# Performance work log

Hardware: AMD Instinct MI355X
Metric: run time of the kernel (lower is better)

Reference implementation:

```python
import jax, jax.numpy as jnp
import numpy as np

B, N, D_IN, D_OUT = 4, 2048, 1024, 1024


def setup_inputs() -> dict:
    key = jax.random.key(0)
    kx, kq, kk, kv = jax.random.split(key, 4)
    x = jax.random.normal(kx, (B, N, D_IN), dtype=jnp.float32)
    # torch Linear(d_in, d_out, bias=False): y = x @ W.T, W ~ U(-1/sqrt(d_in), 1/sqrt(d_in)).
    # Store as [d_in, d_out] so y = x @ W.
    bound = 1.0 / np.sqrt(D_IN)
    Wq = jax.random.uniform(kq, (D_IN, D_OUT), jnp.float32, -bound, bound)
    Wk = jax.random.uniform(kk, (D_IN, D_OUT), jnp.float32, -bound, bound)
    Wv = jax.random.uniform(kv, (D_IN, D_OUT), jnp.float32, -bound, bound)
    return {"x": x, "Wq": Wq, "Wk": Wk, "Wv": Wv}


def reference(x, Wq, Wk, Wv):
    # x: [B, N, d_in]
    q = jnp.einsum("bnd,de->bne", x, Wq)  # [B, N, d_out]
    k = jnp.einsum("bnd,de->bne", x, Wk)
    v = jnp.einsum("bnd,de->bne", x, Wv)
    n = x.shape[1]
    scores = jnp.einsum("bqe,bke->bqk", q, k)  # [B, N, N]
    causal = jnp.triu(jnp.ones((n, n), dtype=bool), k=1)  # True above diagonal -> masked
    scores = jnp.where(causal, -jnp.inf, scores)
    scale = 1.0 / jnp.sqrt(jnp.asarray(k.shape[-1], dtype=scores.dtype))
    weights = jax.nn.softmax(scores * scale, axis=-1)
    # dropout with drop_rate=0.0 is identity
    return jnp.einsum("bqk,bke->bqe", weights, v)  # [B, N, d_out]
```

## Files before the change

kernel.cpp:

```cpp
#include <hip/hip_runtime.h>

typedef float  f4v  __attribute__((ext_vector_type(4)));
typedef short  s8v  __attribute__((ext_vector_type(8)));

__device__ __forceinline__ ushort f2b(float f) {
    union { float f; unsigned int u; } v; v.f = f;
    unsigned int u = v.u;
    u += 0x7fffu + ((u >> 16) & 1u);
    return (ushort)(u >> 16);
}
__device__ __forceinline__ float b2f(ushort u) {
    union { unsigned int u; float f; } v; v.u = ((unsigned int)u) << 16;
    return v.f;
}

__device__ __forceinline__ void async16(const ushort* g, ushort* ldsp) {
    __builtin_amdgcn_global_load_lds(
        (const __attribute__((address_space(1))) unsigned int*)g,
        (__attribute__((address_space(3))) unsigned int*)ldsp, 16, 0, 0);
}

__global__ __launch_bounds__(256) void cast_f32_bf16(const float* __restrict__ in,
                                                     ushort* __restrict__ out,
                                                     float* __restrict__ l, int n4) {
    int i = blockIdx.x * 256 + threadIdx.x;
    if (i < 8192) l[i] = 0.f;
    if (i < n4) {
        float4 f = ((const float4*)in)[i];
        ushort4 o;
        o.x = f2b(f.x); o.y = f2b(f.y); o.z = f2b(f.z); o.w = f2b(f.w);
        ((ushort4*)out)[i] = o;
    }
}

__global__ __launch_bounds__(256) void transpose_cast(const float* __restrict__ w0,
                                                      const float* __restrict__ w1,
                                                      const float* __restrict__ w2,
                                                      ushort* __restrict__ out) {
    __shared__ float tile[32][33];
    const float* W = (blockIdx.z == 0) ? w0 : (blockIdx.z == 1 ? w1 : w2);
    ushort* O = out + (size_t)blockIdx.z * (1024u * 1024u);
    int x0 = blockIdx.x * 32, y0 = blockIdx.y * 32;
    int tx = threadIdx.x, ty = threadIdx.y;
    for (int i = 0; i < 4; i++)
        tile[ty + i * 8][tx] = W[(size_t)(y0 + ty + i * 8) * 1024 + x0 + tx];
    __syncthreads();
    for (int i = 0; i < 4; i++)
        O[(size_t)(x0 + ty + i * 8) * 1024 + y0 + tx] = f2b(tile[tx][ty + i * 8]);
}

#define GEMM_KLOOP64_N64(ArowP_, BrowP_, strideA_, strideB_, K0_, KMAX_)              \
    for (int k0 = (K0_); k0 < (KMAX_); k0 += 64) {                                    \
        async16(ArowP_ + k0, sAw);                                                    \
        async16(ArowP_ + k0 + 16 * (strideA_), sAw + 16 * 32);                        \
        async16(ArowP_ + k0 + 32, sAw + 4096);                                        \
        async16(ArowP_ + k0 + 32 + 16 * (strideA_), sAw + 4096 + 16 * 32);            \
        async16(BrowP_ + k0, sBw);                                                    \
        async16(BrowP_ + k0 + 32, sBw + 2048);                                        \
        __syncthreads();                                                              \
        for (int s = 0; s < 2; s++) {                                                 \
            s8v af[4], bf[2];                                                         \
            for (int mi = 0; mi < 4; mi++)                                            \
                af[mi] = *(const s8v*)&sA[s * 4096 + (wm + mi * 16 + l16) * 32 + quad * 8]; \
            for (int ni = 0; ni < 2; ni++)                                            \
                bf[ni] = *(const s8v*)&sB[s * 2048 + (wn + ni * 16 + l16) * 32 + quad * 8]; \
            for (int mi = 0; mi < 4; mi++)                                            \
                for (int ni = 0; ni < 2; ni++)                                        \
                    acc[mi][ni] = __builtin_amdgcn_mfma_f32_16x16x32_bf16(            \
                        af[mi], bf[ni], acc[mi][ni], 0, 0, 0);                        \
        }                                                                             \
        __syncthreads();                                                              \
    }

#define GEMM_PREAMBLE_N64                                                             \
    const int tid = threadIdx.x;                                                      \
    const int w = tid >> 6, lane = tid & 63, quad = lane >> 4, l16 = lane & 15;       \
    const int wm = (w >> 1) * 64, wn = (w & 1) * 32;                                  \
    f4v acc[4][2];                                                                    \
    for (int mi = 0; mi < 4; mi++)                                                    \
        for (int ni = 0; ni < 2; ni++) acc[mi][ni] = 0;                               \
    ushort* sAw = &sA[(w * 32) * 32];                                                 \
    ushort* sBw = &sB[(w * 16) * 32];

__global__ __launch_bounds__(512, 2) void gemm_qkv(const ushort* __restrict__ A,
                                                   const ushort* __restrict__ Wt,
                                                   ushort* __restrict__ q,
                                                   ushort* __restrict__ k,
                                                   ushort* __restrict__ vt) {
    constexpr int K = 1024;
    extern __shared__ ushort lds[];

    const int L = blockIdx.x;
    const int xcd = L & 7, idx = L >> 3;
    const int ci = xcd >> 1, cj = xcd & 1;
    const int mo = idx / 12, no = idx - mo * 12;
    const int mt = ci * 8 + mo;
    const int ntile = cj * 12 + no;
    const int z = ntile >> 3;
    const int m0 = mt * 256;
    const int n0 = (ntile & 7) * 128;
    const ushort* Bt = Wt + (size_t)z * 1024 * 1024;

    const int tid = threadIdx.x;
    const int w = tid >> 6, lane = tid & 63, quad = lane >> 4, l16 = lane & 15;
    const int wm = (w >> 1) * 64, wn = (w & 1) * 64;

    ushort* a0 = lds;           ushort* b0 = lds + 16384;
    ushort* a1 = lds + 24576;   ushort* b1 = lds + 40960;
    ushort* a2 = lds + 49152;   ushort* b2 = lds + 65536;

    const int lr = lane >> 3;
    const int lc8 = (lane & 7) ^ lr;
    const ushort* Ab = A  + (size_t)(m0 + w * 8 + lr) * K + lc8 * 8;
    const ushort* Bb = Bt + (size_t)(n0 + w * 8 + lr) * K + lc8 * 8;
    const int dW = w * 512;

    f4v acc[4][4];
    #pragma unroll
    for (int mi = 0; mi < 4; mi++)
        #pragma unroll
        for (int ni = 0; ni < 4; ni++) acc[mi][ni] = 0;

    #pragma unroll
    for (int a = 0; a < 4; a++) async16(Ab + (size_t)a * 64 * K,      a0 + a * 4096 + dW);
    #pragma unroll
    for (int b = 0; b < 2; b++) async16(Bb + (size_t)b * 64 * K,      b0 + b * 4096 + dW);
    #pragma unroll
    for (int a = 0; a < 4; a++) async16(Ab + (size_t)a * 64 * K + 64, a1 + a * 4096 + dW);
    #pragma unroll
    for (int b = 0; b < 2; b++) async16(Bb + (size_t)b * 64 * K + 64, b1 + b * 4096 + dW);
    asm volatile("s_waitcnt vmcnt(6)" ::: "memory");
    asm volatile("s_barrier" ::: "memory");

    for (int t = 0; t < 16; ++t) {
        const int k2 = (t + 2) * 64;
        s8v af[4][2], bf[2][2];

        #pragma unroll
        for (int mi = 0; mi < 4; mi++)
            #pragma unroll
            for (int s = 0; s < 2; s++)
                af[mi][s] = *(const s8v*)&a0[(wm + mi * 16 + l16) * 64 +
                                             (((s * 4 + quad) ^ (l16 & 7)) * 8)];
        #pragma unroll
        for (int ni = 0; ni < 2; ni++)
            #pragma unroll
            for (int s = 0; s < 2; s++)
                bf[ni][s] = *(const s8v*)&b0[(wn + ni * 16 + l16) * 64 +
                                             (((s * 4 + quad) ^ (l16 & 7)) * 8)];
        if (t < 14) {
            async16(Ab + (size_t)0 * 64 * K + k2, a2 + 0 * 4096 + dW);
            async16(Ab + (size_t)1 * 64 * K + k2, a2 + 1 * 4096 + dW);
            async16(Ab + (size_t)2 * 64 * K + k2, a2 + 2 * 4096 + dW);
        }
        asm volatile("s_barrier" ::: "memory");
        __builtin_amdgcn_s_setprio(1);
        #pragma unroll
        for (int mi = 0; mi < 4; mi++)
            #pragma unroll
            for (int ni = 0; ni < 2; ni++)
                #pragma unroll
                for (int s = 0; s < 2; s++)
                    acc[mi][ni] = __builtin_amdgcn_mfma_f32_16x16x32_bf16(
                        af[mi][s], bf[ni][s], acc[mi][ni], 0, 0, 0);
        __builtin_amdgcn_s_setprio(0);
        asm volatile("s_barrier" ::: "memory");

        #pragma unroll
        for (int ni = 0; ni < 2; ni++)
            #pragma unroll
            for (int s = 0; s < 2; s++)
                bf[ni][s] = *(const s8v*)&b0[(wn + (ni + 2) * 16 + l16) * 64 +
                                             (((s * 4 + quad) ^ (l16 & 7)) * 8)];
        if (t < 14) {
            async16(Ab + (size_t)3 * 64 * K + k2, a2 + 3 * 4096 + dW);
            async16(Bb + (size_t)0 * 64 * K + k2, b2 + 0 * 4096 + dW);
            async16(Bb + (size_t)1 * 64 * K + k2, b2 + 1 * 4096 + dW);
        }
        asm volatile("s_barrier" ::: "memory");
        __builtin_amdgcn_s_setprio(1);
        #pragma unroll
        for (int mi = 0; mi < 4; mi++)
            #pragma unroll
            for (int ni = 0; ni < 2; ni++)
                #pragma unroll
                for (int s = 0; s < 2; s++)
                    acc[mi][ni + 2] = __builtin_amdgcn_mfma_f32_16x16x32_bf16(
                        af[mi][s], bf[ni][s], acc[mi][ni + 2], 0, 0, 0);
        __builtin_amdgcn_s_setprio(0);

        if (t < 14)       asm volatile("s_waitcnt vmcnt(6)" ::: "memory");
        else if (t == 14) asm volatile("s_waitcnt vmcnt(0)" ::: "memory");
        asm volatile("s_barrier" ::: "memory");

        ushort* ta = a0; a0 = a1; a1 = a2; a2 = ta;
        ushort* tb = b0; b0 = b1; b1 = b2; b2 = tb;
    }

    if (z < 2) {
        ushort* C = (z == 0) ? q : k;
        #pragma unroll
        for (int mi = 0; mi < 4; mi++)
            #pragma unroll
            for (int ni = 0; ni < 4; ni++) {
                int row = m0 + wm + mi * 16 + quad * 4;
                int col = n0 + wn + ni * 16 + l16;
                f4v v = acc[mi][ni];
                #pragma unroll
                for (int rr = 0; rr < 4; rr++)
                    C[(size_t)(row + rr) * 1024 + col] = f2b(v[rr]);
            }
    } else {
        #pragma unroll
        for (int mi = 0; mi < 4; mi++)
            #pragma unroll
            for (int ni = 0; ni < 4; ni++) {
                int row = m0 + wm + mi * 16 + quad * 4;
                int col = n0 + wn + ni * 16 + l16;
                f4v v = acc[mi][ni];
                int b = row >> 11, tok = row & 2047;
                ushort4 pk;
                pk.x = f2b(v[0]); pk.y = f2b(v[1]); pk.z = f2b(v[2]); pk.w = f2b(v[3]);
                *(ushort4*)&vt[(size_t)b * (1024u * 2048u) + (size_t)col * 2048 + tok] = pk;
            }
    }
}

__global__ __launch_bounds__(256) void sgemm_qk(const ushort* __restrict__ Q,
                                                const ushort* __restrict__ Km,
                                                ushort* __restrict__ E,
                                                float* __restrict__ l) {
    constexpr int K = 1024;
    __shared__ ushort sA[2 * 4096];
    __shared__ ushort sB[2 * 2048];
    const int L = blockIdx.x;
    const int t = (L & 7) * 136 + (L >> 3);
    const int b = t / 272;
    const int tt = t - b * 272;
    int mt = 0;
    while ((mt + 1) * (mt + 2) <= tt) mt++;
    const int nt = tt - mt * (mt + 1);
    const ushort* A  = Q  + (size_t)b * 2048 * 1024;
    const ushort* Bt = Km + (size_t)b * 2048 * 1024;
    ushort* C = E + (size_t)b * 2048 * 2048;
    float* lb = l + (size_t)b * 2048;
    const int m0 = mt * 128, n0 = nt * 64;
    GEMM_PREAMBLE_N64
    const ushort* ArowP = A + (size_t)(m0 + w * 32 + (lane >> 2)) * K + (lane & 3) * 8;
    const ushort* BrowP = Bt + (size_t)(n0 + w * 16 + (lane >> 2)) * K + (lane & 3) * 8;
    GEMM_KLOOP64_N64(ArowP, BrowP, K, K, 0, K)

    for (int mi = 0; mi < 4; mi++) {
        for (int rr = 0; rr < 4; rr++) {
            const int row = m0 + wm + mi * 16 + quad * 4 + rr;
            float s = 0.f;
            for (int ni = 0; ni < 2; ni++) {
                int col = n0 + wn + ni * 16 + l16;
                float e = (col <= row) ? __expf(acc[mi][ni][rr] * 0.03125f) : 0.f;
                ushort eb = f2b(e);
                C[(size_t)row * 2048 + col] = eb;
                s += b2f(eb);
            }
            s += __shfl_xor(s, 1);
            s += __shfl_xor(s, 2);
            s += __shfl_xor(s, 4);
            s += __shfl_xor(s, 8);
            if (l16 == 0) atomicAdd(&lb[row], s);
        }
    }
}

__global__ __launch_bounds__(256) void gemm_pv(const ushort* __restrict__ Em,
                                               const ushort* __restrict__ Vt,
                                               const float* __restrict__ l,
                                               float* __restrict__ Out) {
    __shared__ ushort sA[2 * 4096];
    __shared__ ushort sB[2 * 2048];
    const int L = blockIdx.x;
    const int t = (L & 7) * 128 + (L >> 3);
    const int b = t >> 8;
    const int r = t & 255;
    const int qq = r >> 4;
    const int nt = r & 15;
    const int mt = (qq & 1) ? (qq >> 1) : (15 - (qq >> 1));
    const ushort* A  = Em + (size_t)b * 2048 * 2048;
    const ushort* Bt = Vt + (size_t)b * 1024 * 2048;
    const float* lb = l + (size_t)b * 2048;
    float* C = Out + (size_t)b * 2048 * 1024;
    const int m0 = mt * 128, n0 = nt * 64;
    const int Kmax = m0 + 128;
    GEMM_PREAMBLE_N64
    const ushort* ArowP = A + (size_t)(m0 + w * 32 + (lane >> 2)) * 2048 + (lane & 3) * 8;
    const ushort* BrowP = Bt + (size_t)(n0 + w * 16 + (lane >> 2)) * 2048 + (lane & 3) * 8;
    GEMM_KLOOP64_N64(ArowP, BrowP, 2048, 2048, 0, Kmax)

    for (int mi = 0; mi < 4; mi++) {
        const int row = m0 + wm + mi * 16 + quad * 4;
        float inv[4];
        for (int rr = 0; rr < 4; rr++) inv[rr] = 1.f / lb[row + rr];
        for (int ni = 0; ni < 2; ni++) {
            int col = n0 + wn + ni * 16 + l16;
            f4v v = acc[mi][ni];
            for (int rr = 0; rr < 4; rr++)
                C[(size_t)(row + rr) * 1024 + col] = v[rr] * inv[rr];
        }
    }
}

extern "C" void kernel_launch(void* const* d_in, const int* in_sizes, int n_in,
                              void* d_out, int out_size, void* d_ws, size_t ws_size,
                              hipStream_t stream) {
    const float* x  = (const float*)d_in[0];
    const float* Wq = (const float*)d_in[1];
    const float* Wk = (const float*)d_in[2];
    const float* Wv = (const float*)d_in[3];
    float* out = (float*)d_out;

    static bool init = false;
    if (!init) {
        hipFuncSetAttribute(reinterpret_cast<const void*>(gemm_qkv),
                            hipFuncAttributeMaxDynamicSharedMemorySize, 147456);
        init = true;
    }

    char* ws = (char*)d_ws;
    const size_t MiB = 1u << 20;
    ushort* xb = (ushort*)(ws);
    ushort* wt = (ushort*)(ws + 16 * MiB);
    ushort* q  = (ushort*)(ws + 22 * MiB);
    ushort* k  = (ushort*)(ws + 38 * MiB);
    ushort* vt = (ushort*)(ws + 54 * MiB);
    ushort* E  = (ushort*)(ws + 70 * MiB);
    float*  l  = (float*)(ws + 102 * MiB);

    cast_f32_bf16<<<(8192 * 1024 / 4) / 256, 256, 0, stream>>>(x, xb, l, 8192 * 1024 / 4);
    transpose_cast<<<dim3(32, 32, 3), dim3(32, 8), 0, stream>>>(Wq, Wk, Wv, wt);

    gemm_qkv<<<768, 512, 147456, stream>>>(xb, wt, q, k, vt);
    sgemm_qk<<<1088, 256, 0, stream>>>(q, k, E, l);
    gemm_pv<<<1024, 256, 0, stream>>>(E, vt, l, out);
}
```

Before: 232.1 us.

## Widen QKV GEMM tiles to 256x192 with triple-buffered A, double-buffered B

The fused QKV projection GEMM now uses 256x192 output tiles instead of 256x128, which cuts the grid from 768 to 512 blocks, one wave's worth on 256 CUs at 2 blocks per CU. This avoids a partial second wave and raises arithmetic intensity per block. A stays triple-buffered while B is double-buffered with a shorter prefetch distance, and the loads are spread over three MFMA phases. Tiles can now cross the Q/K/V boundary, so the epilogue picks the destination per column. B has less latency slack, and the extra accumulators increase register pressure.

```diff
diff --git a/kernel.cpp b/kernel.cpp
--- a/kernel.cpp
+++ b/kernel.cpp
@@ -93,137 +93,135 @@
     const int L = blockIdx.x;
     const int xcd = L & 7, idx = L >> 3;
     const int ci = xcd >> 1, cj = xcd & 1;
-    const int mo = idx / 12, no = idx - mo * 12;
-    const int mt = ci * 8 + mo;
-    const int ntile = cj * 12 + no;
-    const int z = ntile >> 3;
-    const int m0 = mt * 256;
-    const int n0 = (ntile & 7) * 128;
-    const ushort* Bt = Wt + (size_t)z * 1024 * 1024;
+    const int mo = idx >> 3, no = idx & 7;
+    const int m0 = (ci * 8 + mo) * 256;
+    const int n0 = (cj * 8 + no) * 192;
 
     const int tid = threadIdx.x;
     const int w = tid >> 6, lane = tid & 63, quad = lane >> 4, l16 = lane & 15;
-    const int wm = (w >> 1) * 64, wn = (w & 1) * 64;
-
-    ushort* a0 = lds;           ushort* b0 = lds + 16384;
-    ushort* a1 = lds + 24576;   ushort* b1 = lds + 40960;
-    ushort* a2 = lds + 49152;   ushort* b2 = lds + 65536;
+    const int wm = (w >> 1) * 64, wn = (w & 1) * 96;
+
+    ushort* a0 = lds;
+    ushort* a1 = lds + 16384;
+    ushort* a2 = lds + 32768;
+    ushort* b0 = lds + 49152;
+    ushort* b1 = lds + 61440;
 
     const int lr = lane >> 3;
     const int lc8 = (lane & 7) ^ lr;
     const ushort* Ab = A  + (size_t)(m0 + w * 8 + lr) * K + lc8 * 8;
-    const ushort* Bb = Bt + (size_t)(n0 + w * 8 + lr) * K + lc8 * 8;
+    const ushort* Bb = Wt + (size_t)(n0 + w * 8 + lr) * K + lc8 * 8;
     const int dW = w * 512;
 
-    f4v acc[4][4];
+#define ISSUE_A(buf_, kk_, a_) async16(Ab + (size_t)(a_) * 64 * K + (kk_), (buf_) + (a_) * 4096 + dW)
+#define ISSUE_B(buf_, kk_, c_) async16(Bb + (size_t)(c_) * 64 * K + (kk_), (buf_) + (c_) * 4096 + dW)
+
+#define RD_A(buf_)                                                                    \
+    _Pragma("unroll") for (int mi = 0; mi < 4; mi++)                                  \
+    _Pragma("unroll") for (int s = 0; s < 2; s++)                                     \
+        af[mi][s] = *(const s8v*)&(buf_)[(wm + mi * 16 + l16) * 64 +                  \
+                                         (((s * 4 + quad) ^ (l16 & 7)) * 8)];
+
+#define RD_B2(buf_, NI0_)                                                             \
+    _Pragma("unroll") for (int j = 0; j < 2; j++)                                     \
+    _Pragma("unroll") for (int s = 0; s < 2; s++)                                     \
+        bf[j][s] = *(const s8v*)&(buf_)[(wn + ((NI0_) + j) * 16 + l16) * 64 +         \
+                                        (((s * 4 + quad) ^ (l16 & 7)) * 8)];
+
+#define MFMA16(NI0_)                                                                  \
+    _Pragma("unroll") for (int mi = 0; mi < 4; mi++)                                  \
+    _Pragma("unroll") for (int j = 0; j < 2; j++)                                     \
+    _Pragma("unroll") for (int s = 0; s < 2; s++)                                     \
+        acc[mi][(NI0_) + j] = __builtin_amdgcn_mfma_f32_16x16x32_bf16(                \
+            af[mi][s], bf[j][s], acc[mi][(NI0_) + j], 0, 0, 0);
+
+    f4v acc[4][6];
     #pragma unroll
     for (int mi = 0; mi < 4; mi++)
         #pragma unroll
-        for (int ni = 0; ni < 4; ni++) acc[mi][ni] = 0;
-
-    #pragma unroll
-    for (int a = 0; a < 4; a++) async16(Ab + (size_t)a * 64 * K,      a0 + a * 4096 + dW);
-    #pragma unroll
-    for (int b = 0; b < 2; b++) async16(Bb + (size_t)b * 64 * K,      b0 + b * 4096 + dW);
-    #pragma unroll
-    for (int a = 0; a < 4; a++) async16(Ab + (size_t)a * 64 * K + 64, a1 + a * 4096 + dW);
-    #pragma unroll
-    for (int b = 0; b < 2; b++) async16(Bb + (size_t)b * 64 * K + 64, b1 + b * 4096 + dW);
-    asm volatile("s_waitcnt vmcnt(6)" ::: "memory");
+        for (int ni = 0; ni < 6; ni++) acc[mi][ni] = 0;
+
+    #pragma unroll
+    for (int a = 0; a < 4; a++) ISSUE_A(a0, 0, a);
+    #pragma unroll
+    for (int c = 0; c < 3; c++) ISSUE_B(b0, 0, c);
+    #pragma unroll
+    for (int a = 0; a < 4; a++) ISSUE_A(a1, 64, a);
+    asm volatile("s_waitcnt vmcnt(4)" ::: "memory");
     asm volatile("s_barrier" ::: "memory");
 
     for (int t = 0; t < 16; ++t) {
-        const int k2 = (t + 2) * 64;
+        const int kB = (t + 1) * 64;
+        const int kA = (t + 2) * 64;
         s8v af[4][2], bf[2][2];
 
+        RD_A(a0)
+        RD_B2(b0, 0)
+        if (t < 15) {
+            ISSUE_B(b1, kB, 0);
+            ISSUE_B(b1, kB, 1);
+            ISSUE_B(b1, kB, 2);
+        }
+        asm volatile("s_barrier" ::: "memory");
+        __builtin_amdgcn_s_setprio(1);
+        MFMA16(0)
+        __builtin_amdgcn_s_setprio(0);
+        asm volatile("s_barrier" ::: "memory");
+
+        RD_B2(b0, 2)
+        if (t < 14) {
+            ISSUE_A(a2, kA, 0);
+            ISSUE_A(a2, kA, 1);
+        }
+        asm volatile("s_barrier" ::: "memory");
+        __builtin_amdgcn_s_setprio(1);
+        MFMA16(2)
+        __builtin_amdgcn_s_setprio(0);
+        asm volatile("s_barrier" ::: "memory");
+
+        RD_B2(b0, 4)
+        if (t < 14) {
+            ISSUE_A(a2, kA, 2);
+            ISSUE_A(a2, kA, 3);
+        }
+        asm volatile("s_barrier" ::: "memory");
+        __builtin_amdgcn_s_setprio(1);
+        MFMA16(4)
+        __builtin_amdgcn_s_setprio(0);
+
+        if (t < 14)       asm volatile("s_waitcnt vmcnt(4)" ::: "memory");
+        else if (t == 14) asm volatile("s_waitcnt vmcnt(0)" ::: "memory");
+        asm volatile("s_barrier" ::: "memory");
+
+        ushort* ta = a0; a0 = a1; a1 = a2; a2 = ta;
+        ushort* tb = b0; b0 = b1; b1 = tb;
+    }
+
+    #pragma unroll
+    for (int mi = 0; mi < 4; mi++)
         #pragma unroll
-        for (int mi = 0; mi < 4; mi++)
-            #pragma unroll
-            for (int s = 0; s < 2; s++)
-                af[mi][s] = *(const s8v*)&a0[(wm + mi * 16 + l16) * 64 +
-                                             (((s * 4 + quad) ^ (l16 & 7)) * 8)];
-        #pragma unroll
-        for (int ni = 0; ni < 2; ni++)
-            #pragma unroll
-            for (int s = 0; s < 2; s++)
-                bf[ni][s] = *(const s8v*)&b0[(wn + ni * 16 + l16) * 64 +
-                                             (((s * 4 + quad) ^ (l16 & 7)) * 8)];
-        if (t < 14) {
-            async16(Ab + (size_t)0 * 64 * K + k2, a2 + 0 * 4096 + dW);
-            async16(Ab + (size_t)1 * 64 * K + k2, a2 + 1 * 4096 + dW);
-            async16(Ab + (size_t)2 * 64 * K + k2, a2 + 2 * 4096 + dW);
-        }
-        asm volatile("s_barrier" ::: "memory");
-        __builtin_amdgcn_s_setprio(1);
-        #pragma unroll
-        for (int mi = 0; mi < 4; mi++)
-            #pragma unroll
-            for (int ni = 0; ni < 2; ni++)
-                #pragma unroll
-                for (int s = 0; s < 2; s++)
-                    acc[mi][ni] = __builtin_amdgcn_mfma_f32_16x16x32_bf16(
-                        af[mi][s], bf[ni][s], acc[mi][ni], 0, 0, 0);
-        __builtin_amdgcn_s_setprio(0);
-        asm volatile("s_barrier" ::: "memory");
-
-        #pragma unroll
-        for (int ni = 0; ni < 2; ni++)
-            #pragma unroll
-            for (int s = 0; s < 2; s++)
-                bf[ni][s] = *(const s8v*)&b0[(wn + (ni + 2) * 16 + l16) * 64 +
-                                             (((s * 4 + quad) ^ (l16 & 7)) * 8)];
-        if (t < 14) {
-            async16(Ab + (size_t)3 * 64 * K + k2, a2 + 3 * 4096 + dW);
-            async16(Bb + (size_t)0 * 64 * K + k2, b2 + 0 * 4096 + dW);
-            async16(Bb + (size_t)1 * 64 * K + k2, b2 + 1 * 4096 + dW);
-        }
-        asm volatile("s_barrier" ::: "memory");
-        __builtin_amdgcn_s_setprio(1);
-        #pragma unroll
-        for (int mi = 0; mi < 4; mi++)
-            #pragma unroll
-            for (int ni = 0; ni < 2; ni++)
-                #pragma unroll
-                for (int s = 0; s < 2; s++)
-                    acc[mi][ni + 2] = __builtin_amdgcn_mfma_f32_16x16x32_bf16(
-                        af[mi][s], bf[ni][s], acc[mi][ni + 2], 0, 0, 0);
-        __builtin_amdgcn_s_setprio(0);
-
-        if (t < 14)       asm volatile("s_waitcnt vmcnt(6)" ::: "memory");
-        else if (t == 14) asm volatile("s_waitcnt vmcnt(0)" ::: "memory");
-        asm volatile("s_barrier" ::: "memory");
-
-        ushort* ta = a0; a0 = a1; a1 = a2; a2 = ta;
-        ushort* tb = b0; b0 = b1; b1 = b2; b2 = tb;
-    }
-
-    if (z < 2) {
-        ushort* C = (z == 0) ? q : k;
-        #pragma unroll
-        for (int mi = 0; mi < 4; mi++)
-            #pragma unroll
-            for (int ni = 0; ni < 4; ni++) {
-                int row = m0 + wm + mi * 16 + quad * 4;
-                int col = n0 + wn + ni * 16 + l16;
-                f4v v = acc[mi][ni];
+        for (int ni = 0; ni < 6; ni++) {
+            int row = m0 + wm + mi * 16 + quad * 4;
+            int col = n0 + wn + ni * 16 + l16;
+            int z = col >> 10, cz = col & 1023;
+            f4v v = acc[mi][ni];
+            if (z < 2) {
+                ushort* C = (z == 0) ? q : k;
                 #pragma unroll
                 for (int rr = 0; rr < 4; rr++)
-                    C[(size_t)(row + rr) * 1024 + col] = f2b(v[rr]);
-            }
-    } else {
-        #pragma unroll
-        for (int mi = 0; mi < 4; mi++)
-            #pragma unroll
-            for (int ni = 0; ni < 4; ni++) {
-                int row = m0 + wm + mi * 16 + quad * 4;
-                int col = n0 + wn + ni * 16 + l16;
-                f4v v = acc[mi][ni];
+                    C[(size_t)(row + rr) * 1024 + cz] = f2b(v[rr]);
+            } else {
                 int b = row >> 11, tok = row & 2047;
                 ushort4 pk;
                 pk.x = f2b(v[0]); pk.y = f2b(v[1]); pk.z = f2b(v[2]); pk.w = f2b(v[3]);
-                *(ushort4*)&vt[(size_t)b * (1024u * 2048u) + (size_t)col * 2048 + tok] = pk;
+                *(ushort4*)&vt[(size_t)b * (1024u * 2048u) + (size_t)cz * 2048 + tok] = pk;
             }
-    }
+        }
+#undef ISSUE_A
+#undef ISSUE_B
+#undef RD_A
+#undef RD_B2
+#undef MFMA16
 }
 
 __global__ __launch_bounds__(256) void sgemm_qk(const ushort* __restrict__ Q,
@@ -336,7 +334,7 @@
     cast_f32_bf16<<<(8192 * 1024 / 4) / 256, 256, 0, stream>>>(x, xb, l, 8192 * 1024 / 4);
     transpose_cast<<<dim3(32, 32, 3), dim3(32, 8), 0, stream>>>(Wq, Wk, Wv, wt);
 
-    gemm_qkv<<<768, 512, 147456, stream>>>(xb, wt, q, k, vt);
+    gemm_qkv<<<512, 512, 147456, stream>>>(xb, wt, q, k, vt);
     sgemm_qk<<<1088, 256, 0, stream>>>(q, k, E, l);
     gemm_pv<<<1024, 256, 0, stream>>>(E, vt, l, out);
 }
```

After: 222.5 us. -4.1%, faster.
